# Kernel tuning notes

Measured on AMD Instinct MI355X. Metric: run time of the kernel, lower is better.

## Reference

```python
import jax, jax.numpy as jnp
import numpy as np

N_HEADS = 16


def setup_inputs() -> dict:
    key = jax.random.key(0)
    ks = jax.random.split(key, 5)
    B, S, D = 2, 2048, 1024
    x = jax.random.normal(ks[0], (B, S, D), dtype=jnp.float32)
    Wqkv = jax.random.normal(ks[1], (D, 3 * D), dtype=jnp.float32) * (1.0 / np.sqrt(D))
    bqkv = jax.random.normal(ks[2], (3 * D,), dtype=jnp.float32) * 0.02
    Wout = jax.random.normal(ks[3], (D, D), dtype=jnp.float32) * (1.0 / np.sqrt(D))
    bout = jax.random.normal(ks[4], (D,), dtype=jnp.float32) * 0.02
    return {"x": x, "Wqkv": Wqkv, "bqkv": bqkv, "Wout": Wout, "bout": bout}


def reference(x, Wqkv, bqkv, Wout, bout):
    B, S, D = x.shape
    H = N_HEADS
    dh = D // H
    # qkv projection, then view as [B,S,H,3*dh] and chunk on last dim
    # (matches torch: per-head q/k/v are interleaved slices of the projection)
    qkv = (x @ Wqkv + bqkv).reshape(B, S, H, 3 * dh).transpose(0, 2, 1, 3)  # [B,H,S,3dh]
    q, k, v = jnp.split(qkv, 3, axis=-1)  # each [B,H,S,dh]
    scale = jnp.asarray(1.0 / np.sqrt(dh), dtype=x.dtype)
    scores = jnp.einsum('bhqd,bhkd->bhqk', q, k) * scale  # [B,H,S,S]
    causal = jnp.tril(jnp.ones((S, S), dtype=bool))
    scores = jnp.where(causal, scores, jnp.asarray(-jnp.inf, dtype=scores.dtype))
    attn_w = jax.nn.softmax(scores, axis=-1)
    attn = jnp.einsum('bhqk,bhkd->bhqd', attn_w, v)  # [B,H,S,dh]
    attn = attn.transpose(0, 2, 1, 3).reshape(B, S, D)
    return attn @ Wout + bout
```

## Files before the change

kernel.cpp:

```cpp
#include <hip/hip_runtime.h>
#include <hip/hip_bf16.h>
#include <cstdint>
#include <cstddef>

typedef __hip_bfloat16 bf16;
typedef short bf16x4 __attribute__((ext_vector_type(4)));
typedef short bf16x8 __attribute__((ext_vector_type(8)));
typedef float f32x4 __attribute__((ext_vector_type(4)));

#define LOG2E 1.44269504088896f

static constexpr int Bb = 2, S = 2048, D = 1024, H = 16, DH = 64;

struct TrueT  { static constexpr bool value = true;  };
struct FalseT { static constexpr bool value = false; };

__device__ inline short f2bf_bits(float f) {
  bf16 b = __float2bfloat16(f);
  short s;
  __builtin_memcpy(&s, &b, 2);
  return s;
}
__device__ inline float bfbits2f(short s) {
  uint32_t u = ((uint32_t)(uint16_t)s) << 16;
  float f;
  __builtin_memcpy(&f, &u, 4);
  return f;
}

__global__ __launch_bounds__(256) void prep_kernel(
    const float* __restrict__ Wqkv, bf16* __restrict__ wqkvT,
    const float* __restrict__ Wout, bf16* __restrict__ woutT,
    const float* __restrict__ x, bf16* __restrict__ xbf) {
  const int blk = blockIdx.x;
  const int tid = threadIdx.x;
  if (blk < 4096) {
    __shared__ float t[32][33];
    const float* in;
    bf16* out;
    int R, C, bx, by;
    if (blk < 3072) { in = Wqkv; out = wqkvT; R = 1024; C = 3072; bx = blk % 96; by = blk / 96; }
    else            { in = Wout; out = woutT; R = 1024; C = 1024; bx = (blk - 3072) % 32; by = (blk - 3072) / 32; }
    int c0 = bx * 32, r0 = by * 32;
    int tx = tid & 31, ty = tid >> 5;
#pragma unroll
    for (int i = 0; i < 4; i++) {
      int r = ty + i * 8;
      t[r][tx] = in[(size_t)(r0 + r) * C + c0 + tx];
    }
    __syncthreads();
#pragma unroll
    for (int i = 0; i < 4; i++) {
      int c = ty + i * 8;
      out[(size_t)(c0 + c) * R + r0 + tx] = __float2bfloat16(t[tx][c]);
    }
  } else {
    size_t i = ((size_t)(blk - 4096) * 256 + tid) * 8;
    f32x4 a = *(const f32x4*)(x + i);
    f32x4 b = *(const f32x4*)(x + i + 4);
    bf16x8 v;
#pragma unroll
    for (int j = 0; j < 4; j++) { v[j] = f2bf_bits(a[j]); v[4 + j] = f2bf_bits(b[j]); }
    *(bf16x8*)((short*)xbf + i) = v;
  }
}

__global__ __launch_bounds__(256) void gemm_qkv(
    const bf16* __restrict__ A, const bf16* __restrict__ Bt,
    const float* __restrict__ bias,
    bf16* __restrict__ Qb, bf16* __restrict__ Kb, bf16* __restrict__ Vtb) {
  constexpr int K = 1024;
  __shared__ __align__(16) short smA[128 * 32];
  __shared__ __align__(16) short smB[128 * 32];
  __shared__ __align__(16) short smE[4][16 * 72];

  const int tid = threadIdx.x;
  const int wave = tid >> 6, lane = tid & 63;
  const int quad = lane >> 4, l16 = lane & 15;
  const int m0 = blockIdx.y * 128, n0 = blockIdx.x * 128;
  const int wm = wave >> 1, wn = wave & 1;

  f32x4 acc[4][4];
#pragma unroll
  for (int i = 0; i < 4; i++)
#pragma unroll
    for (int j = 0; j < 4; j++) acc[i][j] = {0.f, 0.f, 0.f, 0.f};

  const int srow = lane >> 2;
  const int scol = (lane & 3) * 8;

  for (int k0 = 0; k0 < K; k0 += 32) {
#pragma unroll
    for (int half = 0; half < 2; half++) {
      int row = half * 64 + wave * 16 + srow;
      const bf16* ga = A + (size_t)(m0 + row) * K + k0 + scol;
      const bf16* gb = Bt + (size_t)(n0 + row) * K + k0 + scol;
      __builtin_amdgcn_global_load_lds(
          (const __attribute__((address_space(1))) void*)ga,
          (__attribute__((address_space(3))) void*)&smA[(half * 64 + wave * 16) * 32],
          16, 0, 0);
      __builtin_amdgcn_global_load_lds(
          (const __attribute__((address_space(1))) void*)gb,
          (__attribute__((address_space(3))) void*)&smB[(half * 64 + wave * 16) * 32],
          16, 0, 0);
    }
    __syncthreads();

    bf16x8 af[4], bf_[4];
#pragma unroll
    for (int mi = 0; mi < 4; mi++)
      af[mi] = *(const bf16x8*)&smA[(wm * 64 + mi * 16 + l16) * 32 + quad * 8];
#pragma unroll
    for (int ni = 0; ni < 4; ni++)
      bf_[ni] = *(const bf16x8*)&smB[(wn * 64 + ni * 16 + l16) * 32 + quad * 8];
#pragma unroll
    for (int mi = 0; mi < 4; mi++)
#pragma unroll
      for (int ni = 0; ni < 4; ni++)
        acc[mi][ni] = __builtin_amdgcn_mfma_f32_16x16x32_bf16(
            af[mi], bf_[ni], acc[mi][ni], 0, 0, 0);
    __syncthreads();
  }

  const int cs0 = n0 + wn * 64;
  const int h = cs0 / 192;
  const int rt = (cs0 >> 6) % 3;
  const int t0w = m0 + wm * 64;
  const int b = t0w >> 11, s0w = t0w & 2047;

  float bv[4];
#pragma unroll
  for (int ni = 0; ni < 4; ni++) bv[ni] = bias[cs0 + ni * 16 + l16];

  if (rt < 2) {
    const float qscale = (rt == 0) ? (0.125f * LOG2E) : 1.0f;
    bf16* dst = (rt == 0 ? Qb : Kb) + ((size_t)(b * H + h) * S + s0w) * 64;
    short* sE = &smE[wave][0];
    const int r8 = lane >> 2, s4 = lane & 3;
#pragma unroll
    for (int mi = 0; mi < 4; mi++) {
#pragma unroll
      for (int ni = 0; ni < 4; ni++)
#pragma unroll
        for (int r = 0; r < 4; r++)
          sE[(quad * 4 + r) * 72 + ni * 16 + l16] =
              f2bf_bits((acc[mi][ni][r] + bv[ni]) * qscale);
      asm volatile("s_waitcnt lgkmcnt(0)" ::: "memory");
      bf16x8 w0 = *(const bf16x8*)&sE[r8 * 72 + s4 * 16];
      bf16x8 w1 = *(const bf16x8*)&sE[r8 * 72 + s4 * 16 + 8];
      short* g = (short*)dst + (size_t)(mi * 16 + r8) * 64 + s4 * 16;
      *(bf16x8*)g = w0;
      *(bf16x8*)(g + 8) = w1;
      asm volatile("s_waitcnt lgkmcnt(0)" ::: "memory");
    }
  } else {
#pragma unroll
    for (int ni = 0; ni < 4; ni++) {
      const int dh = ni * 16 + l16;
#pragma unroll
      for (int mi = 0; mi < 4; mi++) {
        const int s0 = s0w + mi * 16 + quad * 4;
        size_t base = ((size_t)(b * H + h) * 64 + dh) * S + s0;
        bf16x4 vv;
#pragma unroll
        for (int r = 0; r < 4; r++) vv[r] = f2bf_bits(acc[mi][ni][r] + bv[ni]);
        *(bf16x4*)((short*)Vtb + base) = vv;
      }
    }
  }
}

__global__ __launch_bounds__(256) void gemm_out(
    const bf16* __restrict__ A, const bf16* __restrict__ Bt,
    const float* __restrict__ bias, float* __restrict__ C,
    int M, int N, int K) {
  constexpr int BN = 64, NF = 2;
  __shared__ __align__(16) short smA[128 * 32];
  __shared__ __align__(16) short smB[BN * 32];
  __shared__ __align__(16) float smEf[4][580];

  const int tid = threadIdx.x;
  const int wave = tid >> 6, lane = tid & 63;
  const int quad = lane >> 4, l16 = lane & 15;
  const int m0 = blockIdx.y * 128, n0 = blockIdx.x * BN;
  const int wm = wave >> 1, wn = wave & 1;

  f32x4 acc[4][NF];
#pragma unroll
  for (int i = 0; i < 4; i++)
#pragma unroll
    for (int j = 0; j < NF; j++) acc[i][j] = {0.f, 0.f, 0.f, 0.f};

  const int srow = lane >> 2;
  const int scol = (lane & 3) * 8;

  for (int k0 = 0; k0 < K; k0 += 32) {
#pragma unroll
    for (int half = 0; half < 2; half++) {
      int row = half * 64 + wave * 16 + srow;
      const bf16* ga = A + (size_t)(m0 + row) * K + k0 + scol;
      __builtin_amdgcn_global_load_lds(
          (const __attribute__((address_space(1))) void*)ga,
          (__attribute__((address_space(3))) void*)&smA[(half * 64 + wave * 16) * 32],
          16, 0, 0);
    }
    {
      int row = wave * 16 + srow;
      const bf16* gb = Bt + (size_t)(n0 + row) * K + k0 + scol;
      __builtin_amdgcn_global_load_lds(
          (const __attribute__((address_space(1))) void*)gb,
          (__attribute__((address_space(3))) void*)&smB[(wave * 16) * 32],
          16, 0, 0);
    }
    __syncthreads();

    bf16x8 af[4], bf_[NF];
#pragma unroll
    for (int mi = 0; mi < 4; mi++)
      af[mi] = *(const bf16x8*)&smA[(wm * 64 + mi * 16 + l16) * 32 + quad * 8];
#pragma unroll
    for (int ni = 0; ni < NF; ni++)
      bf_[ni] = *(const bf16x8*)&smB[(wn * 32 + ni * 16 + l16) * 32 + quad * 8];
#pragma unroll
    for (int mi = 0; mi < 4; mi++)
#pragma unroll
      for (int ni = 0; ni < NF; ni++)
        acc[mi][ni] = __builtin_amdgcn_mfma_f32_16x16x32_bf16(
            af[mi], bf_[ni], acc[mi][ni], 0, 0, 0);
    __syncthreads();
  }

  float bv[NF];
#pragma unroll
  for (int ni = 0; ni < NF; ni++) bv[ni] = bias[n0 + wn * 32 + ni * 16 + l16];

  float* sE = &smEf[wave][0];
#pragma unroll
  for (int mi = 0; mi < 4; mi++) {
#pragma unroll
    for (int ni = 0; ni < NF; ni++)
#pragma unroll
      for (int r = 0; r < 4; r++)
        sE[(quad * 4 + r) * 36 + ni * 16 + l16] = acc[mi][ni][r] + bv[ni];
    asm volatile("s_waitcnt lgkmcnt(0)" ::: "memory");
#pragma unroll
    for (int t = 0; t < 2; t++) {
      int slot = t * 64 + lane;
      int rr = slot >> 3, c4 = slot & 7;
      f32x4 v = *(const f32x4*)&sE[rr * 36 + c4 * 4];
      int row = m0 + wm * 64 + mi * 16 + rr;
      int col = n0 + wn * 32 + c4 * 4;
      *(f32x4*)&C[(size_t)row * N + col] = v;
    }
    asm volatile("s_waitcnt lgkmcnt(0)" ::: "memory");
  }
}

__global__ __launch_bounds__(256) void attn_kernel(
    const bf16* __restrict__ Qb, const bf16* __restrict__ Kb,
    const bf16* __restrict__ Vtb,
    bf16* __restrict__ Op0, bf16* __restrict__ Op1, bf16* __restrict__ Op2,
    float* __restrict__ lp0, float* __restrict__ lp1, float* __restrict__ lp2,
    bf16* __restrict__ Ofinal, int split) {
  const int blk = blockIdx.x;
  int sk, p, bh;
  if (split == 3)      { sk = blk % 3; int r = blk / 3; p = r & 15; bh = r >> 4; }
  else if (split == 2) { sk = blk & 1; p = (blk >> 1) & 15; bh = blk >> 5; }
  else                 { sk = 0;       p = blk & 15;        bh = blk >> 4; }
  const int h = bh & (H - 1), b = bh >> 4;
  const int tid = threadIdx.x;
  const int wave = tid >> 6, lane = tid & 63;
  const int quad = lane >> 4, l16 = lane & 15;

  bf16*  __restrict__ Op = (sk == 0) ? Op0 : (sk == 1) ? Op1 : Op2;
  float* __restrict__ lp = (sk == 0) ? lp0 : (sk == 1) ? lp1 : lp2;

  const bf16* Qh = Qb + (size_t)(b * H + h) * S * 64;
  const bf16* Kh = Kb + (size_t)(b * H + h) * S * 64;
  const bf16* Vth = Vtb + (size_t)(b * H + h) * 64 * S;

  __shared__ __align__(16) short smK[64 * 64];
  __shared__ __align__(16) short smVt[64 * 64];
  __shared__ __align__(16) short pLds[4][16][76];

  const int lrow = lane >> 3;
  const int lg = lane & 7;
  const int swz = l16 & 7;

  bf16x8 onesB;
#pragma unroll
  for (int j = 0; j < 8; j++) onesB[j] = (short)0x3F80;

#pragma unroll
  for (int pass = 0; pass < 2; pass++) {
    const int qt = pass ? p : (31 - p);
    const int q0 = qt * 64 + wave * 16;
    const int qglob = q0 + l16;

    bf16x8 aQ[2];
#pragma unroll
    for (int kh = 0; kh < 2; kh++)
      aQ[kh] = *(const bf16x8*)(Qh + (size_t)(q0 + l16) * 64 + kh * 32 + quad * 8);

    f32x4 o[4];
#pragma unroll
    for (int dt = 0; dt < 4; dt++) o[dt] = {0.f, 0.f, 0.f, 0.f};
    f32x4 lacc = {0.f, 0.f, 0.f, 0.f};

    auto tile = [&](int it, auto diag_tag) {
      constexpr bool DIAG = decltype(diag_tag)::value;
      const int kv0 = it * 64;
      __syncthreads();

#pragma unroll
      for (int j = 0; j < 2; j++) {
        const int row = wave * 16 + j * 8 + lrow;
        const bf16* ks = Kh + (size_t)(kv0 + row) * 64 + (lg ^ (row & 7)) * 8;
        __builtin_amdgcn_global_load_lds(
            (const __attribute__((address_space(1))) void*)ks,
            (__attribute__((address_space(3))) void*)&smK[(wave * 16 + j * 8) * 64],
            16, 0, 0);
        const bf16* vs = Vth + (size_t)row * S + kv0 + (lg ^ (row & 7)) * 8;
        __builtin_amdgcn_global_load_lds(
            (const __attribute__((address_space(1))) void*)vs,
            (__attribute__((address_space(3))) void*)&smVt[(wave * 16 + j * 8) * 64],
            16, 0, 0);
      }
      __syncthreads();

      f32x4 z[4];
#pragma unroll
      for (int nh = 0; nh < 4; nh++) {
        const int row = nh * 16 + l16;
        f32x4 t = {0.f, 0.f, 0.f, 0.f};
#pragma unroll
        for (int kh = 0; kh < 2; kh++) {
          bf16x8 bK = *(const bf16x8*)&smK[row * 64 + ((kh * 4 + quad) ^ swz) * 8];
          t = __builtin_amdgcn_mfma_f32_16x16x32_bf16(bK, aQ[kh], t, 0, 0, 0);
        }
        z[nh] = t;
      }

#pragma unroll
      for (int nh = 0; nh < 4; nh++) {
        bf16x4 pk;
#pragma unroll
        for (int r = 0; r < 4; r++) {
          float e = exp2f(z[nh][r]);
          if (DIAG) {
            const int kidx = kv0 + nh * 16 + quad * 4 + r;
            e = (kidx <= qglob) ? e : 0.f;
          }
          pk[r] = f2bf_bits(e);
        }
        *(bf16x4*)&pLds[wave][l16][nh * 16 + quad * 4] = pk;
      }

      asm volatile("s_waitcnt lgkmcnt(0)" ::: "memory");

      bf16x8 aP[2];
#pragma unroll
      for (int k2 = 0; k2 < 2; k2++)
        aP[k2] = *(const bf16x8*)&pLds[wave][l16][k2 * 32 + quad * 8];
#pragma unroll
      for (int k2 = 0; k2 < 2; k2++)
        lacc = __builtin_amdgcn_mfma_f32_16x16x32_bf16(aP[k2], onesB, lacc, 0, 0, 0);
#pragma unroll
      for (int dt = 0; dt < 4; dt++) {
        const int row = dt * 16 + l16;
#pragma unroll
        for (int k2 = 0; k2 < 2; k2++) {
          bf16x8 bV = *(const bf16x8*)&smVt[row * 64 + ((k2 * 4 + quad) ^ swz) * 8];
          o[dt] = __builtin_amdgcn_mfma_f32_16x16x32_bf16(aP[k2], bV, o[dt], 0, 0, 0);
        }
      }
    };

    int it = sk;
    for (; it < qt; it += split) tile(it, FalseT{});
    if (it == qt) tile(qt, TrueT{});

    if (split > 1) {
      const size_t rowbase = (size_t)(b * H + h) * S + q0;
      if (l16 == 0) {
#pragma unroll
        for (int r = 0; r < 4; r++) lp[rowbase + quad * 4 + r] = lacc[r];
      }
#pragma unroll
      for (int r = 0; r < 4; r++) {
        const size_t row = rowbase + quad * 4 + r;
#pragma unroll
        for (int dt = 0; dt < 4; dt++)
          ((short*)Op)[row * 64 + dt * 16 + l16] = f2bf_bits(o[dt][r]);
      }
    } else {
#pragma unroll
      for (int r = 0; r < 4; r++) {
        const float inv = 1.f / lacc[r];
        const int q = q0 + quad * 4 + r;
#pragma unroll
        for (int dt = 0; dt < 4; dt++)
          Ofinal[(size_t)(b * S + q) * D + h * 64 + dt * 16 + l16] =
              __float2bfloat16(o[dt][r] * inv);
      }
    }
  }
}

__global__ __launch_bounds__(256) void attn_reduce(
    const bf16* __restrict__ O0, const bf16* __restrict__ O1,
    const bf16* __restrict__ O2,
    const float* __restrict__ l0, const float* __restrict__ l1,
    const float* __restrict__ l2,
    bf16* __restrict__ attnO, int nparts) {
  int gid = blockIdx.x * 256 + threadIdx.x;
  int row = gid >> 3;
  int c8 = (gid & 7) * 8;
  float lsum = l0[row] + l1[row];
  if (nparts == 3) lsum += l2[row];
  float inv = 1.f / lsum;
  bf16x8 a = *(const bf16x8*)((const short*)O0 + (size_t)row * 64 + c8);
  bf16x8 bb = *(const bf16x8*)((const short*)O1 + (size_t)row * 64 + c8);
  float acc[8];
#pragma unroll
  for (int j = 0; j < 8; j++) acc[j] = bfbits2f(a[j]) + bfbits2f(bb[j]);
  if (nparts == 3) {
    bf16x8 c = *(const bf16x8*)((const short*)O2 + (size_t)row * 64 + c8);
#pragma unroll
    for (int j = 0; j < 8; j++) acc[j] += bfbits2f(c[j]);
  }
  bf16x8 o;
#pragma unroll
  for (int j = 0; j < 8; j++) o[j] = f2bf_bits(acc[j] * inv);
  int bh = row >> 11, q = row & 2047;
  int b = bh >> 4, h = bh & 15;
  *(bf16x8*)((short*)attnO + (((size_t)(b * S + q) * H + h) * 64 + c8)) = o;
}

extern "C" void kernel_launch(void* const* d_in, const int* in_sizes, int n_in,
                              void* d_out, int out_size, void* d_ws, size_t ws_size,
                              hipStream_t stream) {
  const float* x    = (const float*)d_in[0];
  const float* Wqkv = (const float*)d_in[1];
  const float* bqkv = (const float*)d_in[2];
  const float* Wout = (const float*)d_in[3];
  const float* bout = (const float*)d_in[4];
  float* out = (float*)d_out;

  char* ws = (char*)d_ws;
  int split;
  if (ws_size >= 59506688)      split = 3;
  else if (ws_size >= 50855936) split = 2;
  else                          split = 1;

  bf16* Qb  = (bf16*)(ws);
  bf16* Kb  = (bf16*)(ws + 8388608);
  bf16* Vtb = (bf16*)(ws + 16777216);
  bf16* xbf = (bf16*)(ws + 25165824);

  bf16 *Op0 = nullptr, *Op1 = nullptr, *Op2 = nullptr, *attnO;
  float *lp0 = nullptr, *lp1 = nullptr, *lp2 = nullptr;
  bf16 *wqkvT, *woutT;
  if (split == 3) {
    Op0   = (bf16*)(ws + 25165824);
    Op1   = (bf16*)(ws + 33554432);
    Op2   = (bf16*)(ws + 41943040);
    lp0   = (float*)(ws + 50331648);
    lp1   = (float*)(ws + 50593792);
    lp2   = (float*)(ws + 50855936);
    attnO = (bf16*)(ws + 8388608);
    wqkvT = (bf16*)(ws + 51118080);
    woutT = (bf16*)(ws + 57409536);
  } else if (split == 2) {
    Op0   = (bf16*)(ws + 25165824);
    Op1   = (bf16*)(ws + 33554432);
    lp0   = (float*)(ws + 41943040);
    lp1   = (float*)(ws + 42205184);
    attnO = (bf16*)(ws + 8388608);
    wqkvT = (bf16*)(ws + 42467328);
    woutT = (bf16*)(ws + 48758784);
  } else {
    attnO = (bf16*)(ws + 25165824);
    wqkvT = (bf16*)(ws + 33554432);
    woutT = (bf16*)(ws + 39845888);
  }

  prep_kernel<<<dim3(6144), 256, 0, stream>>>(Wqkv, wqkvT, Wout, woutT, x, xbf);

  gemm_qkv<<<dim3(3072 / 128, 4096 / 128), 256, 0, stream>>>(
      xbf, wqkvT, bqkv, Qb, Kb, Vtb);

  if (split == 3) {
    attn_kernel<<<dim3(1536), 256, 0, stream>>>(
        Qb, Kb, Vtb, Op0, Op1, Op2, lp0, lp1, lp2, nullptr, 3);
    attn_reduce<<<dim3(2048), 256, 0, stream>>>(Op0, Op1, Op2, lp0, lp1, lp2, attnO, 3);
  } else if (split == 2) {
    attn_kernel<<<dim3(1024), 256, 0, stream>>>(
        Qb, Kb, Vtb, Op0, Op1, Op0, lp0, lp1, lp0, nullptr, 2);
    attn_reduce<<<dim3(2048), 256, 0, stream>>>(Op0, Op1, Op0, lp0, lp1, lp0, attnO, 2);
  } else {
    attn_kernel<<<dim3(512), 256, 0, stream>>>(
        Qb, Kb, Vtb, nullptr, nullptr, nullptr, nullptr, nullptr, nullptr, attnO, 1);
  }

  gemm_out<<<dim3(1024 / 64, 4096 / 128), 256, 0, stream>>>(
      attnO, woutT, bout, out, 4096, 1024, 1024);
}
```

Measured before the change: 192.3 us.

## Register-prefetch next K/V tile during compute and remap blocks across XCDs

Replaces the direct global-to-LDS loads, which were issued and then waited on before each tile, with register prefetch of the next K/V tile. Those loads are issued before the current tile's MFMA work and written to LDS afterwards, so global latency overlaps compute. Blocks are also remapped so that all blocks of one (batch, head) land on the same XCD for L2 reuse, and launch bounds request higher occupancy. The trade-off is more register pressure and LDS store instructions, with the K/V swizzle now applied on the LDS write.

```diff
diff --git a/kernel.cpp b/kernel.cpp
--- a/kernel.cpp
+++ b/kernel.cpp
@@ -7,6 +7,7 @@
 typedef short bf16x4 __attribute__((ext_vector_type(4)));
 typedef short bf16x8 __attribute__((ext_vector_type(8)));
 typedef float f32x4 __attribute__((ext_vector_type(4)));
+typedef int i32x4 __attribute__((ext_vector_type(4)));
 
 #define LOG2E 1.44269504088896f
 
@@ -256,17 +257,19 @@
   }
 }
 
-__global__ __launch_bounds__(256) void attn_kernel(
+__global__ __launch_bounds__(256, 6) void attn_kernel(
     const bf16* __restrict__ Qb, const bf16* __restrict__ Kb,
     const bf16* __restrict__ Vtb,
     bf16* __restrict__ Op0, bf16* __restrict__ Op1, bf16* __restrict__ Op2,
     float* __restrict__ lp0, float* __restrict__ lp1, float* __restrict__ lp2,
     bf16* __restrict__ Ofinal, int split) {
   const int blk = blockIdx.x;
+  const int xcd = blk & 7;
+  const int idx = blk >> 3;
   int sk, p, bh;
-  if (split == 3)      { sk = blk % 3; int r = blk / 3; p = r & 15; bh = r >> 4; }
-  else if (split == 2) { sk = blk & 1; p = (blk >> 1) & 15; bh = blk >> 5; }
-  else                 { sk = 0;       p = blk & 15;        bh = blk >> 4; }
+  if (split == 3)      { bh = xcd + 8 * (idx / 48); int r = idx % 48; p = r & 15; sk = r >> 4; }
+  else if (split == 2) { bh = xcd + 8 * (idx / 32); int r = idx % 32; p = r & 15; sk = r >> 4; }
+  else                 { bh = xcd + 8 * (idx / 16); p = idx & 15; sk = 0; }
   const int h = bh & (H - 1), b = bh >> 4;
   const int tid = threadIdx.x;
   const int wave = tid >> 6, lane = tid & 63;
@@ -287,6 +290,11 @@
   const int lg = lane & 7;
   const int swz = l16 & 7;
 
+  const int row0 = wave * 16 + lrow;
+  const int row1 = wave * 16 + 8 + lrow;
+  const int col0 = (lg ^ (row0 & 7)) * 8;
+  const int col1 = (lg ^ (row1 & 7)) * 8;
+
   bf16x8 onesB;
 #pragma unroll
   for (int j = 0; j < 8; j++) onesB[j] = (short)0x3F80;
@@ -307,26 +315,25 @@
     for (int dt = 0; dt < 4; dt++) o[dt] = {0.f, 0.f, 0.f, 0.f};
     f32x4 lacc = {0.f, 0.f, 0.f, 0.f};
 
-    auto tile = [&](int it, auto diag_tag) {
+    i32x4 kreg0, kreg1, vreg0, vreg1;
+
+    auto issue_loads = [&](int it2) {
+      const int kv0 = it2 * 64;
+      kreg0 = *(const i32x4*)(Kh + (size_t)(kv0 + row0) * 64 + col0);
+      vreg0 = *(const i32x4*)(Vth + (size_t)row0 * S + kv0 + col0);
+      kreg1 = *(const i32x4*)(Kh + (size_t)(kv0 + row1) * 64 + col1);
+      vreg1 = *(const i32x4*)(Vth + (size_t)row1 * S + kv0 + col1);
+    };
+    auto write_lds = [&]() {
+      *(i32x4*)&smK[row0 * 64 + lg * 8] = kreg0;
+      *(i32x4*)&smVt[row0 * 64 + lg * 8] = vreg0;
+      *(i32x4*)&smK[row1 * 64 + lg * 8] = kreg1;
+      *(i32x4*)&smVt[row1 * 64 + lg * 8] = vreg1;
+    };
+
+    auto compute_tile = [&](int it2, auto diag_tag) {
       constexpr bool DIAG = decltype(diag_tag)::value;
-      const int kv0 = it * 64;
-      __syncthreads();
-
-#pragma unroll
-      for (int j = 0; j < 2; j++) {
-        const int row = wave * 16 + j * 8 + lrow;
-        const bf16* ks = Kh + (size_t)(kv0 + row) * 64 + (lg ^ (row & 7)) * 8;
-        __builtin_amdgcn_global_load_lds(
-            (const __attribute__((address_space(1))) void*)ks,
-            (__attribute__((address_space(3))) void*)&smK[(wave * 16 + j * 8) * 64],
-            16, 0, 0);
-        const bf16* vs = Vth + (size_t)row * S + kv0 + (lg ^ (row & 7)) * 8;
-        __builtin_amdgcn_global_load_lds(
-            (const __attribute__((address_space(1))) void*)vs,
-            (__attribute__((address_space(3))) void*)&smVt[(wave * 16 + j * 8) * 64],
-            16, 0, 0);
-      }
-      __syncthreads();
+      const int kv0 = it2 * 64;
 
       f32x4 z[4];
 #pragma unroll
@@ -377,8 +384,24 @@
     };
 
     int it = sk;
-    for (; it < qt; it += split) tile(it, FalseT{});
-    if (it == qt) tile(qt, TrueT{});
+    const bool have0 = (it <= qt);
+    if (have0) issue_loads(it);
+    __syncthreads();
+    if (have0) write_lds();
+    __syncthreads();
+    while (it <= qt) {
+      const int next = it + split;
+      const bool hn = (next <= qt);
+      if (hn) issue_loads(next);
+      if (it == qt) compute_tile(it, TrueT{});
+      else          compute_tile(it, FalseT{});
+      if (hn) {
+        __syncthreads();
+        write_lds();
+        __syncthreads();
+      }
+      it = next;
+    }
 
     if (split > 1) {
       const size_t rowbase = (size_t)(b * H + h) * S + q0;
```

Measured after the change: 389.8 us. +102.7%, slower.

## Double-buffer K/V tiles in attention and remap blocks to XCDs by head

Applied to the files above, without the earlier changes.

The attention kernel now stages K and V^T tiles into two LDS buffers. The next tile's global-to-LDS load is issued before the current tile is computed, which should overlap memory latency with MFMA work and removes one barrier per tile. Block indices are also remapped so that all blocks of the same batch-head land on the same XCD (blk & 7), aiming to improve L2 reuse of K/V. LDS use for K/V doubles, which may lower occupancy. Correctness relies on the async LDS loads completing before the trailing __syncthreads.

```diff
diff --git a/kernel.cpp b/kernel.cpp
--- a/kernel.cpp
+++ b/kernel.cpp
@@ -263,10 +263,12 @@
     float* __restrict__ lp0, float* __restrict__ lp1, float* __restrict__ lp2,
     bf16* __restrict__ Ofinal, int split) {
   const int blk = blockIdx.x;
+  const int xcd = blk & 7;
+  const int idx = blk >> 3;
   int sk, p, bh;
-  if (split == 3)      { sk = blk % 3; int r = blk / 3; p = r & 15; bh = r >> 4; }
-  else if (split == 2) { sk = blk & 1; p = (blk >> 1) & 15; bh = blk >> 5; }
-  else                 { sk = 0;       p = blk & 15;        bh = blk >> 4; }
+  if (split == 3)      { bh = xcd + 8 * (idx / 48); int r = idx % 48; p = r & 15; sk = r >> 4; }
+  else if (split == 2) { bh = xcd + 8 * (idx / 32); int r = idx % 32; p = r & 15; sk = r >> 4; }
+  else                 { bh = xcd + 8 * (idx / 16); p = idx & 15; sk = 0; }
   const int h = bh & (H - 1), b = bh >> 4;
   const int tid = threadIdx.x;
   const int wave = tid >> 6, lane = tid & 63;
@@ -279,8 +281,8 @@
   const bf16* Kh = Kb + (size_t)(b * H + h) * S * 64;
   const bf16* Vth = Vtb + (size_t)(b * H + h) * 64 * S;
 
-  __shared__ __align__(16) short smK[64 * 64];
-  __shared__ __align__(16) short smVt[64 * 64];
+  __shared__ __align__(16) short smK[2][64 * 64];
+  __shared__ __align__(16) short smVt[2][64 * 64];
   __shared__ __align__(16) short pLds[4][16][76];
 
   const int lrow = lane >> 3;
@@ -290,6 +292,24 @@
   bf16x8 onesB;
 #pragma unroll
   for (int j = 0; j < 8; j++) onesB[j] = (short)0x3F80;
+
+  auto stage = [&](int it2, int bufi) {
+    const int kv0 = it2 * 64;
+#pragma unroll
+    for (int j = 0; j < 2; j++) {
+      const int row = wave * 16 + j * 8 + lrow;
+      const bf16* ks = Kh + (size_t)(kv0 + row) * 64 + (lg ^ (row & 7)) * 8;
+      __builtin_amdgcn_global_load_lds(
+          (const __attribute__((address_space(1))) void*)ks,
+          (__attribute__((address_space(3))) void*)&smK[bufi][(wave * 16 + j * 8) * 64],
+          16, 0, 0);
+      const bf16* vs = Vth + (size_t)row * S + kv0 + (lg ^ (row & 7)) * 8;
+      __builtin_amdgcn_global_load_lds(
+          (const __attribute__((address_space(1))) void*)vs,
+          (__attribute__((address_space(3))) void*)&smVt[bufi][(wave * 16 + j * 8) * 64],
+          16, 0, 0);
+    }
+  };
 
 #pragma unroll
   for (int pass = 0; pass < 2; pass++) {
@@ -307,26 +327,9 @@
     for (int dt = 0; dt < 4; dt++) o[dt] = {0.f, 0.f, 0.f, 0.f};
     f32x4 lacc = {0.f, 0.f, 0.f, 0.f};
 
-    auto tile = [&](int it, auto diag_tag) {
+    auto compute_tile = [&](int it2, int bufi, auto diag_tag) {
       constexpr bool DIAG = decltype(diag_tag)::value;
-      const int kv0 = it * 64;
-      __syncthreads();
-
-#pragma unroll
-      for (int j = 0; j < 2; j++) {
-        const int row = wave * 16 + j * 8 + lrow;
-        const bf16* ks = Kh + (size_t)(kv0 + row) * 64 + (lg ^ (row & 7)) * 8;
-        __builtin_amdgcn_global_load_lds(
-            (const __attribute__((address_space(1))) void*)ks,
-            (__attribute__((address_space(3))) void*)&smK[(wave * 16 + j * 8) * 64],
-            16, 0, 0);
-        const bf16* vs = Vth + (size_t)row * S + kv0 + (lg ^ (row & 7)) * 8;
-        __builtin_amdgcn_global_load_lds(
-            (const __attribute__((address_space(1))) void*)vs,
-            (__attribute__((address_space(3))) void*)&smVt[(wave * 16 + j * 8) * 64],
-            16, 0, 0);
-      }
-      __syncthreads();
+      const int kv0 = it2 * 64;
 
       f32x4 z[4];
 #pragma unroll
@@ -335,7 +338,7 @@
         f32x4 t = {0.f, 0.f, 0.f, 0.f};
 #pragma unroll
         for (int kh = 0; kh < 2; kh++) {
-          bf16x8 bK = *(const bf16x8*)&smK[row * 64 + ((kh * 4 + quad) ^ swz) * 8];
+          bf16x8 bK = *(const bf16x8*)&smK[bufi][row * 64 + ((kh * 4 + quad) ^ swz) * 8];
           t = __builtin_amdgcn_mfma_f32_16x16x32_bf16(bK, aQ[kh], t, 0, 0, 0);
         }
         z[nh] = t;
@@ -370,15 +373,26 @@
         const int row = dt * 16 + l16;
 #pragma unroll
         for (int k2 = 0; k2 < 2; k2++) {
-          bf16x8 bV = *(const bf16x8*)&smVt[row * 64 + ((k2 * 4 + quad) ^ swz) * 8];
+          bf16x8 bV = *(const bf16x8*)&smVt[bufi][row * 64 + ((k2 * 4 + quad) ^ swz) * 8];
           o[dt] = __builtin_amdgcn_mfma_f32_16x16x32_bf16(aP[k2], bV, o[dt], 0, 0, 0);
         }
       }
     };
 
     int it = sk;
-    for (; it < qt; it += split) tile(it, FalseT{});
-    if (it == qt) tile(qt, TrueT{});
+    __syncthreads();
+    if (it <= qt) stage(it, 0);
+    __syncthreads();
+    int cur = 0;
+    while (it <= qt) {
+      const int next = it + split;
+      if (next <= qt) stage(next, cur ^ 1);
+      if (it == qt) compute_tile(it, cur, TrueT{});
+      else          compute_tile(it, cur, FalseT{});
+      __syncthreads();
+      cur ^= 1;
+      it = next;
+    }
 
     if (split > 1) {
       const size_t rowbase = (size_t)(b * H + h) * S + q0;
```

Result: no change. 189.4 us (-1.5%).
